# Kernel optimization log

Hardware: AMD Instinct MI355X
Metric: run time of the kernel (lower is better)

## Reference

```python
import jax, jax.numpy as jnp
import numpy as np

# Sizes (see shape_source): N samples, D=Config.dim, H=D//2, E question types, C classes/type
N, D, H, E, C = 65536, 768, 384, 8, 8


def setup_inputs() -> dict:
    key = jax.random.key(0)
    k_x, k_t, k_w1, k_w2 = jax.random.split(key, 4)
    x = jax.random.normal(k_x, (N, D), dtype=jnp.float32)
    question_types = jax.random.randint(k_t, (N,), 0, E, dtype=jnp.int32)
    # Stacked per-type MLP head parameters (E experts)
    W1 = jax.random.normal(k_w1, (E, D, H), dtype=jnp.float32) * 0.02
    b1 = jnp.zeros((E, H), dtype=jnp.float32)
    W2 = jax.random.normal(k_w2, (E, H, C), dtype=jnp.float32) * 0.02
    b2 = jnp.zeros((E, C), dtype=jnp.float32)
    return {"x": x, "W1": W1, "b1": b1, "W2": W2, "b2": b2,
            "question_types": question_types}


def reference(x, W1, b1, W2, b2, question_types):
    # Per-sample routed 2-layer MLP head: logits_i = MLP_{type_i}(x_i).
    # Dropout is eval-mode identity. Dense-per-expert compute + mask select
    # (standard MoE reference; E is a small fixed loop, not a data-dim loop).
    n_experts = W1.shape[0]
    out = jnp.zeros((x.shape[0], W2.shape[-1]), dtype=x.dtype)
    for e in range(n_experts):
        h = jax.nn.relu(x @ W1[e] + b1[e])        # [N, H]
        logits = h @ W2[e] + b2[e]                # [N, C]
        out = jnp.where((question_types == e)[:, None], logits, out)
    return out
```

## Files before the change

### kernel.cpp

```cpp
#include <hip/hip_runtime.h>

typedef short s16x8 __attribute__((ext_vector_type(8)));
typedef float f32x4 __attribute__((ext_vector_type(4)));

#define N_SAMPLES 65536
#define DIM 768
#define HID 384
#define NEXP 8
#define NCLS 8
#define JT 24
#define KT 24

#define WS_CNT    0
#define WS_BUCKET 1024
#define WS_W1F    (WS_BUCKET + NEXP * N_SAMPLES * 4)

__device__ __forceinline__ unsigned short f2bf(float f) {
  union { float f; unsigned u; } v; v.f = f;
  unsigned r = v.u + 0x7fffu + ((v.u >> 16) & 1u);
  return (unsigned short)(r >> 16);
}

__device__ __forceinline__ unsigned cvt2(float a, float b) {
  union { float f; unsigned u; } ua, ub;
  ua.f = a; ub.f = b;
  return __builtin_amdgcn_perm(ub.u + 0x8000u, ua.u + 0x8000u, 0x07060302u);
}

#define LBAR asm volatile("s_waitcnt lgkmcnt(0)\n\ts_barrier" ::: "memory")

__global__ void k_w1frag(const float* __restrict__ W1,
                         unsigned short* __restrict__ W1F,
                         int* __restrict__ cnt) {
  if (blockIdx.x == 0 && blockIdx.y == 0 && threadIdx.x < NEXP)
    cnt[threadIdx.x] = 0;
  const int e = blockIdx.x;
  const int unit = blockIdx.y * 4 + (threadIdx.x >> 6);
  const int lane = threadIdx.x & 63;
  const int jt = unit / KT, kt = unit % KT;
  const int j = jt * 16 + (lane & 15);
  const int k0 = kt * 32 + (lane >> 4) * 8;
  const float* src = W1 + ((size_t)e * DIM + k0) * HID + j;
  s16x8 v;
#pragma unroll
  for (int i = 0; i < 8; ++i) v[i] = (short)f2bf(src[(size_t)i * HID]);
  *(s16x8*)&W1F[(((size_t)e * JT * KT + unit) * 64 + lane) * 8] = v;
}

__global__ void k_scatter(const int* __restrict__ qt, int* __restrict__ cnt,
                          int* __restrict__ bucket) {
  __shared__ int lcnt[NEXP], lbase[NEXP];
  const int t = threadIdx.x;
  const int i = blockIdx.x * 256 + t;
  if (t < NEXP) lcnt[t] = 0;
  __syncthreads();
  const int e = qt[i];
  const int rank = atomicAdd(&lcnt[e], 1);
  __syncthreads();
  if (t < NEXP) lbase[t] = atomicAdd(&cnt[t], lcnt[t]);
  __syncthreads();
  bucket[(size_t)e * N_SAMPLES + lbase[e] + rank] = i;
}

#define ALOAD(LO, HI, KS)                                   \
  { const float4* p_ = (const float4*)(ap + (KS) * 32);     \
    LO = p_[0]; HI = p_[1]; }

#define ASTORE(BUF, LO, HI)                                               \
  { unsigned q0 = cvt2((LO).x, (LO).y), q1 = cvt2((LO).z, (LO).w);        \
    unsigned q2 = cvt2((HI).x, (HI).y), q3 = cvt2((HI).z, (HI).w);        \
    uint4 pk_ = {q0, q1, q2, q3};                                         \
    *(uint4*)&(BUF)[ar * 40 + aq * 8] = pk_; }

#define WLOAD(DST, KS)                                                    \
  _Pragma("unroll") for (int ni = 0; ni < 6; ++ni)                        \
      DST[ni] = *(const s16x8*)(wfbase + ((size_t)ni * KT + (KS)) * 512);

#define COMPUTE(AS, WF)                                                   \
  { _Pragma("unroll") for (int mi = 0; mi < 4; ++mi) {                    \
      s16x8 xfr = *(const s16x8*)&(AS)[(mi * 16 + lrow) * 40 + quad * 8]; \
      _Pragma("unroll") for (int ni = 0; ni < 6; ++ni)                    \
          acc[mi][ni] = __builtin_amdgcn_mfma_f32_16x16x32_bf16(          \
              WF[ni], xfr, acc[mi][ni], 0, 0, 0); } }

__global__ __launch_bounds__(256, 2) void k_moe_gemm(
    const float* __restrict__ x, const unsigned short* __restrict__ W1F,
    const float* __restrict__ b1, const float* __restrict__ W2,
    const float* __restrict__ b2, const int* __restrict__ cnt,
    const int* __restrict__ bucket, float* __restrict__ out) {
  __shared__ __align__(16) short smem[25088];
  __shared__ __align__(16) short W2s[16 * 392];
  __shared__ float b1s[HID];
  __shared__ float b2s[NCLS];
  short* As0 = smem;
  short* As1 = smem + 2560;
  short* Hs  = smem;

  const int e = blockIdx.x;
  const int n_e = cnt[e];
  const int t = threadIdx.x;
  const int lane = t & 63;
  const int wave = t >> 6;
  const int lrow = lane & 15;
  const int quad = lane >> 4;
  const int ar = t >> 2;
  const int aq = t & 3;

  for (int j = t; j < HID; j += 256) {
    b1s[j] = b1[e * HID + j];
    const float* wr = W2 + ((size_t)e * HID + j) * NCLS;
#pragma unroll
    for (int c = 0; c < NCLS; ++c) W2s[c * 392 + j] = (short)f2bf(wr[c]);
#pragma unroll
    for (int c = NCLS; c < 16; ++c) W2s[c * 392 + j] = 0;
  }
  if (t < NCLS) b2s[t] = b2[e * NCLS + t];

  const unsigned short* wfbase =
      W1F + ((size_t)(e * JT + wave * 6) * KT) * 512 + lane * 8;

  for (int rt = blockIdx.y; rt * 64 < n_e; rt += gridDim.y) {
    const int row0 = rt * 64;
    int slot = row0 + ar;
    if (slot >= n_e) slot = n_e - 1;
    const int aidx = bucket[(size_t)e * N_SAMPLES + slot];
    const float* ap = x + (size_t)aidx * DIM + aq * 8;

    f32x4 acc[4][6];
#pragma unroll
    for (int mi = 0; mi < 4; ++mi)
#pragma unroll
      for (int ni = 0; ni < 6; ++ni) acc[mi][ni] = (f32x4){0.f, 0.f, 0.f, 0.f};

    float4 a0lo, a0hi, a1lo, a1hi;
    s16x8 wf0[6], wf1[6];
    ALOAD(a0lo, a0hi, 0)
    ASTORE(As0, a0lo, a0hi)
    ALOAD(a1lo, a1hi, 1)
    WLOAD(wf0, 0)
    LBAR;

    for (int ks = 0; ks < 24; ks += 2) {
      if (ks + 1 < 24) { ASTORE(As1, a1lo, a1hi) WLOAD(wf1, ks + 1) }
      if (ks + 2 < 24) ALOAD(a0lo, a0hi, ks + 2)
      COMPUTE(As0, wf0)
      LBAR;
      if (ks + 2 < 24) { ASTORE(As0, a0lo, a0hi) WLOAD(wf0, ks + 2) }
      if (ks + 3 < 24) ALOAD(a1lo, a1hi, ks + 3)
      COMPUTE(As1, wf1)
      LBAR;
    }

#pragma unroll
    for (int mi = 0; mi < 4; ++mi)
#pragma unroll
      for (int ni = 0; ni < 6; ++ni) {
        const int j = wave * 96 + ni * 16 + quad * 4;
        const float4 bb = *(const float4*)&b1s[j];
        float v0 = acc[mi][ni][0] + bb.x; v0 = v0 > 0.f ? v0 : 0.f;
        float v1 = acc[mi][ni][1] + bb.y; v1 = v1 > 0.f ? v1 : 0.f;
        float v2 = acc[mi][ni][2] + bb.z; v2 = v2 > 0.f ? v2 : 0.f;
        float v3 = acc[mi][ni][3] + bb.w; v3 = v3 > 0.f ? v3 : 0.f;
        uint2 pk = {cvt2(v0, v1), cvt2(v2, v3)};
        *(uint2*)&Hs[(mi * 16 + lrow) * 392 + j] = pk;
      }
    LBAR;

    {
      f32x4 acc2 = (f32x4){0.f, 0.f, 0.f, 0.f};
#pragma unroll
      for (int kk = 0; kk < 12; ++kk) {
        s16x8 af = *(const s16x8*)&Hs[(wave * 16 + lrow) * 392 + kk * 32 + quad * 8];
        s16x8 bf = *(const s16x8*)&W2s[lrow * 392 + kk * 32 + quad * 8];
        acc2 = __builtin_amdgcn_mfma_f32_16x16x32_bf16(af, bf, acc2, 0, 0, 0);
      }
      if (lrow < NCLS) {
        const float bb = b2s[lrow];
#pragma unroll
        for (int r = 0; r < 4; ++r) {
          const int m = wave * 16 + quad * 4 + r;
          if (row0 + m < n_e) {
            const int oi = bucket[(size_t)e * N_SAMPLES + row0 + m];
            out[(size_t)oi * NCLS + lrow] = acc2[r] + bb;
          }
        }
      }
    }
    LBAR;
  }
}

extern "C" void kernel_launch(void* const* d_in, const int* in_sizes, int n_in,
                              void* d_out, int out_size, void* d_ws, size_t ws_size,
                              hipStream_t stream) {
  const float* x  = (const float*)d_in[0];
  const float* W1 = (const float*)d_in[1];
  const float* b1 = (const float*)d_in[2];
  const float* W2 = (const float*)d_in[3];
  const float* b2 = (const float*)d_in[4];
  const int* qt   = (const int*)d_in[5];
  float* out = (float*)d_out;
  char* ws = (char*)d_ws;

  int* cnt = (int*)(ws + WS_CNT);
  int* bucket = (int*)(ws + WS_BUCKET);
  unsigned short* W1F = (unsigned short*)(ws + WS_W1F);

  k_w1frag<<<dim3(8, 144), dim3(256), 0, stream>>>(W1, W1F, cnt);
  k_scatter<<<dim3(256), dim3(256), 0, stream>>>(qt, cnt, bucket);
  k_moe_gemm<<<dim3(8, 64), dim3(256), 0, stream>>>(x, W1F, b1, W2, b2, cnt, bucket, out);
}
```

Measured before the change: 334.3 us.

## Deepen software pipeline for A and W1 fragment loads, prefetch next row indices

Restructures the K loop of the routed MoE GEMM so global loads of x are issued four steps ahead and W1 fragments two steps ahead, using register ring buffers and a fully unrolled loop. It also prefetches the next tile's bucket index before the current tile's compute so the gather address is ready sooner, and adds an early exit for empty experts. The aim is to hide global memory latency better, at the cost of many more live registers under a two-blocks-per-CU launch bound, which could cause spills or lower occupancy.

```diff
diff --git a/kernel.cpp b/kernel.cpp
--- a/kernel.cpp
+++ b/kernel.cpp
@@ -62,26 +62,29 @@
   bucket[(size_t)e * N_SAMPLES + lbase[e] + rank] = i;
 }
 
-#define ALOAD(LO, HI, KS)                                   \
+
+#define ALOADI(SLOT, KS)                                    \
   { const float4* p_ = (const float4*)(ap + (KS) * 32);     \
-    LO = p_[0]; HI = p_[1]; }
-
-#define ASTORE(BUF, LO, HI)                                               \
-  { unsigned q0 = cvt2((LO).x, (LO).y), q1 = cvt2((LO).z, (LO).w);        \
-    unsigned q2 = cvt2((HI).x, (HI).y), q3 = cvt2((HI).z, (HI).w);        \
-    uint4 pk_ = {q0, q1, q2, q3};                                         \
+    aLo[SLOT] = p_[0]; aHi[SLOT] = p_[1]; }
+
+#define ASTOREI(BUF, SLOT)                                                  \
+  { unsigned q0 = cvt2(aLo[SLOT].x, aLo[SLOT].y),                           \
+             q1 = cvt2(aLo[SLOT].z, aLo[SLOT].w),                           \
+             q2 = cvt2(aHi[SLOT].x, aHi[SLOT].y),                           \
+             q3 = cvt2(aHi[SLOT].z, aHi[SLOT].w);                           \
+    uint4 pk_ = {q0, q1, q2, q3};                                           \
     *(uint4*)&(BUF)[ar * 40 + aq * 8] = pk_; }
 
-#define WLOAD(DST, KS)                                                    \
-  _Pragma("unroll") for (int ni = 0; ni < 6; ++ni)                        \
-      DST[ni] = *(const s16x8*)(wfbase + ((size_t)ni * KT + (KS)) * 512);
-
-#define COMPUTE(AS, WF)                                                   \
-  { _Pragma("unroll") for (int mi = 0; mi < 4; ++mi) {                    \
-      s16x8 xfr = *(const s16x8*)&(AS)[(mi * 16 + lrow) * 40 + quad * 8]; \
-      _Pragma("unroll") for (int ni = 0; ni < 6; ++ni)                    \
-          acc[mi][ni] = __builtin_amdgcn_mfma_f32_16x16x32_bf16(          \
-              WF[ni], xfr, acc[mi][ni], 0, 0, 0); } }
+#define WLOADI(SLOT, KS)                                                    \
+  _Pragma("unroll") for (int ni = 0; ni < 6; ++ni)                          \
+      wf[SLOT][ni] = *(const s16x8*)(wfbase + ((size_t)ni * KT + (KS)) * 512);
+
+#define COMPUTEI(AS, SLOT)                                                  \
+  { _Pragma("unroll") for (int mi = 0; mi < 4; ++mi) {                      \
+      s16x8 xfr = *(const s16x8*)&(AS)[(mi * 16 + lrow) * 40 + quad * 8];   \
+      _Pragma("unroll") for (int ni = 0; ni < 6; ++ni)                      \
+          acc[mi][ni] = __builtin_amdgcn_mfma_f32_16x16x32_bf16(            \
+              wf[SLOT][ni], xfr, acc[mi][ni], 0, 0, 0); } }
 
 __global__ __launch_bounds__(256, 2) void k_moe_gemm(
     const float* __restrict__ x, const unsigned short* __restrict__ W1F,
@@ -98,6 +101,7 @@
 
   const int e = blockIdx.x;
   const int n_e = cnt[e];
+  if (n_e <= 0) return;
   const int t = threadIdx.x;
   const int lane = t & 63;
   const int wave = t >> 6;
@@ -119,11 +123,18 @@
   const unsigned short* wfbase =
       W1F + ((size_t)(e * JT + wave * 6) * KT) * 512 + lane * 8;
 
+  int aidx = 0;
+  {
+    const int rt0 = blockIdx.y;
+    if (rt0 * 64 < n_e) {
+      int slot = rt0 * 64 + ar;
+      if (slot >= n_e) slot = n_e - 1;
+      aidx = bucket[(size_t)e * N_SAMPLES + slot];
+    }
+  }
+
   for (int rt = blockIdx.y; rt * 64 < n_e; rt += gridDim.y) {
     const int row0 = rt * 64;
-    int slot = row0 + ar;
-    if (slot >= n_e) slot = n_e - 1;
-    const int aidx = bucket[(size_t)e * N_SAMPLES + slot];
     const float* ap = x + (size_t)aidx * DIM + aq * 8;
 
     f32x4 acc[4][6];
@@ -132,22 +143,32 @@
 #pragma unroll
       for (int ni = 0; ni < 6; ++ni) acc[mi][ni] = (f32x4){0.f, 0.f, 0.f, 0.f};
 
-    float4 a0lo, a0hi, a1lo, a1hi;
-    s16x8 wf0[6], wf1[6];
-    ALOAD(a0lo, a0hi, 0)
-    ASTORE(As0, a0lo, a0hi)
-    ALOAD(a1lo, a1hi, 1)
-    WLOAD(wf0, 0)
+    float4 aLo[4], aHi[4];
+    s16x8 wf[3][6];
+
+    ALOADI(0, 0) ALOADI(1, 1) ALOADI(2, 2) ALOADI(3, 3)
+    WLOADI(0, 0) WLOADI(1, 1)
+    ASTOREI(As0, 0)
+
+    int aidx_n = aidx;
+    {
+      const int nrt = rt + gridDim.y;
+      if (nrt * 64 < n_e) {
+        int s = nrt * 64 + ar;
+        if (s >= n_e) s = n_e - 1;
+        aidx_n = bucket[(size_t)e * N_SAMPLES + s];
+      }
+    }
     LBAR;
 
-    for (int ks = 0; ks < 24; ks += 2) {
-      if (ks + 1 < 24) { ASTORE(As1, a1lo, a1hi) WLOAD(wf1, ks + 1) }
-      if (ks + 2 < 24) ALOAD(a0lo, a0hi, ks + 2)
-      COMPUTE(As0, wf0)
-      LBAR;
-      if (ks + 2 < 24) { ASTORE(As0, a0lo, a0hi) WLOAD(wf0, ks + 2) }
-      if (ks + 3 < 24) ALOAD(a1lo, a1hi, ks + 3)
-      COMPUTE(As1, wf1)
+#pragma unroll
+    for (int ks = 0; ks < 24; ++ks) {
+      short* bufc = (ks & 1) ? As1 : As0;
+      short* bufn = (ks & 1) ? As0 : As1;
+      if (ks + 4 < 24) ALOADI((ks + 4) & 3, ks + 4)
+      if (ks + 2 < 24) WLOADI((ks + 2) % 3, ks + 2)
+      if (ks + 1 < 24) ASTOREI(bufn, (ks + 1) & 3)
+      COMPUTEI(bufc, ks % 3)
       LBAR;
     }
 
@@ -187,6 +208,7 @@
       }
     }
     LBAR;
+    aidx = aidx_n;
   }
 }
 
```

Measured after the change: 461.4 us. +38.0%, slower.
